# Optimization experiments

Hardware: AMD Instinct MI355X
Metric: run time of the kernel (lower is better)

## Reference

```python
import jax, jax.numpy as jnp
import numpy as np

BD = BH = BW = 4  # block sizes
NH = 8            # num heads


def setup_inputs() -> dict:
    key = jax.random.key(0)
    ks = jax.random.split(key, 5)
    C = 128
    return {
        "x": jax.random.normal(ks[0], (1, C, 30, 62, 126), dtype=jnp.float32),
        "qkv_w": jax.random.normal(ks[1], (3 * C, C), dtype=jnp.float32) * 0.02,
        "qkv_b": jax.random.normal(ks[2], (3 * C,), dtype=jnp.float32) * 0.02,
        "conv_w": jax.random.normal(ks[3], (C, C), dtype=jnp.float32) * 0.02,
        "conv_b": jax.random.normal(ks[4], (C,), dtype=jnp.float32) * 0.02,
    }


def reference(x, qkv_w, qkv_b, conv_w, conv_b):
    B, C, D0, H0, W0 = x.shape
    pad_d = (-D0) % BD
    pad_b = (-H0) % BH
    pad_r = (-W0) % BW
    x = jnp.pad(x, ((0, 0), (0, 0), (0, pad_d), (0, pad_b), (0, pad_r)))
    _, _, D, H, W = x.shape
    d, h, w = D // BD, H // BH, W // BW
    nW, L, hd = d * h * w, BD * BH * BW, C // NH
    scale = hd ** -0.5

    # window partition: (B,C,D,H,W) -> (B, nW, L, C)
    xb = x.reshape(B, C, d, BD, h, BH, w, BW).transpose(0, 2, 4, 6, 3, 5, 7, 1)
    xw = xb.reshape(B, nW, L, C)

    qkv = xw @ qkv_w.T + qkv_b                         # (B,nW,L,3C)
    qkv = qkv.reshape(B, nW, L, 3, NH, hd).transpose(3, 0, 1, 4, 2, 5)
    q, k, v = qkv[0], qkv[1], qkv[2]                   # (B,nW,NH,L,hd)

    attn = jnp.einsum('bnhld,bnhmd->bnhlm', q, k) * scale

    if pad_d > 0 or pad_r > 0 or pad_b > 0:
        mask = jnp.zeros((D, H, W), dtype=x.dtype)
        mask = mask.at[-pad_d:, :, :].set(1.0)
        mask = mask.at[:, -pad_b:, :].set(1.0)
        mask = mask.at[:, :, -pad_r:].set(1.0)
        mask = mask.reshape(d, BD, h, BH, w, BW).transpose(0, 2, 4, 1, 3, 5).reshape(nW, L)
        am = mask[:, None, :] - mask[:, :, None]       # (nW,L,L): mask[j]-mask[i]
        am = jnp.where(am != 0, jnp.asarray(-1000.0, x.dtype), jnp.asarray(0.0, x.dtype))
        attn = attn + am[None, :, None, :, :]

    attn = jax.nn.softmax(attn, axis=-1)
    out = jnp.einsum('bnhlm,bnhmd->bnhld', attn, v)    # (B,nW,NH,L,hd)

    # window merge: -> (B,C,D,H,W)
    out = out.reshape(B, d, h, w, NH, BD, BH, BW, hd)
    out = out.transpose(0, 4, 8, 1, 5, 2, 6, 3, 7).reshape(B, C, D, H, W)
    out = out[:, :, :D0, :H0, :W0]

    # final 1x1x1 conv
    out = jnp.einsum('bcdhw,oc->bodhw', out, conv_w) + conv_b[None, :, None, None, None]
    return out
```

## Files before the change

kernel.cpp:

```cpp
#include <hip/hip_runtime.h>


#define NHEAD 8
#define HDIM 16
#define CCH 128
#define DD0 30
#define HH0 62
#define WW0 126
#define SD 7812
#define SC 234360

typedef __bf16 bfx8 __attribute__((ext_vector_type(8)));
typedef float  fx4  __attribute__((ext_vector_type(4)));
typedef float  fx2  __attribute__((ext_vector_type(2)));

__device__ __forceinline__ fx4 MFMA(bfx8 a, bfx8 b, fx4 c) {
    return __builtin_amdgcn_mfma_f32_16x16x32_bf16(a, b, c, 0, 0, 0);
}
__device__ __forceinline__ fx4 fzero4() { fx4 v = {0.f, 0.f, 0.f, 0.f}; return v; }
__device__ __forceinline__ bfx8 bzero8() {
    bfx8 v;
    #pragma unroll
    for (int j = 0; j < 8; j++) v[j] = (__bf16)0.f;
    return v;
}
__device__ __forceinline__ unsigned pk2(float a, float b) {
    __bf16 ax = (__bf16)a, by = (__bf16)b;
    unsigned short ua = __builtin_bit_cast(unsigned short, ax);
    unsigned short ub = __builtin_bit_cast(unsigned short, by);
    return (unsigned)ua | ((unsigned)ub << 16);
}

__global__ void prep_kernel(const float* __restrict__ qkv_w,
                            const float* __restrict__ conv_w,
                            __bf16* __restrict__ Bq, __bf16* __restrict__ Bc) {
    const int i = blockIdx.x * 256 + threadIdx.x;
    if (i < 49152) Bq[i] = (__bf16)qkv_w[i];
    else            Bc[i - 49152] = (__bf16)conv_w[i - 49152];
}

__global__ __launch_bounds__(256, 4) void winattn_kernel(
    const float* __restrict__ x,
    const float* __restrict__ qkv_b,
    const float* __restrict__ conv_b,
    const __bf16* __restrict__ Bq,
    const __bf16* __restrict__ Bc,
    float* __restrict__ out)
{
    __shared__ __align__(16) unsigned char lds_raw[32768];
    __bf16* ldsQ = (__bf16*)lds_raw;
    __bf16* ldsK = (__bf16*)(lds_raw + 16384);

    const int tid  = threadIdx.x;
    const int wave = tid >> 6;
    const int lane = tid & 63;
    const int quad = lane >> 4;
    const int l15  = lane & 15;

    const int blk = blockIdx.x;
    const int wid = ((blk & 7) << 9) | (blk >> 3);
    const int Db = (wid >> 9) << 2;
    const int Hb = ((wid >> 5) & 15) << 2;
    const int Wb = (wid & 31) << 2;

    unsigned long long pmask;
    {
        const bool p = (Db + (lane >> 4) >= DD0) || (Hb + ((lane >> 2) & 3) >= HH0) ||
                       (Wb + (lane & 3) >= WW0);
        pmask = __ballot(p);
    }

    {
        #pragma unroll
        for (int it = 0; it < 16; it++) {
            const int u = it * 256 + tid;
            const int wp = u & 1;
            const int dh = (u >> 1) & 15;
            const int c  = u >> 5;
            const int Dg = Db + (dh >> 2), Hg = Hb + (dh & 3);
            const bool valid = (Dg < DD0) && (Hg < HH0) && (wp == 0 || Wb < 124);
            fx2 v = {0.f, 0.f};
            if (valid) v = *(const fx2*)(x + c * SC + Dg * SD + Hg * WW0 + Wb + wp * 2);
            const int tok0 = dh * 4 + wp * 2;
            ldsQ[tok0 * 128 + (((c >> 3) ^ (tok0 & 15)) << 3) + (c & 7)] = (__bf16)v[0];
            const int tok1 = tok0 + 1;
            ldsQ[tok1 * 128 + (((c >> 3) ^ (tok1 & 15)) << 3) + (c & 7)] = (__bf16)v[1];
        }
    }
    __syncthreads();

    unsigned vpk[2][4][2];

    {
        fx4 acc[4][4];
        #pragma unroll
        for (int mt = 0; mt < 4; mt++)
            #pragma unroll
            for (int j = 0; j < 4; j++) acc[mt][j] = fzero4();
        #pragma unroll
        for (int ks = 0; ks < 4; ks++) {
            bfx8 a[4];
            #pragma unroll
            for (int mt = 0; mt < 4; mt++) {
                const int m = mt * 16 + l15;
                const int phys = (ks * 4 + quad) ^ (m & 15);
                a[mt] = *(const bfx8*)(ldsQ + m * 128 + phys * 8);
            }
            #pragma unroll
            for (int j = 0; j < 4; j++) {
                const int col = (1 + (j >> 1)) * 128 + (wave + (j & 1) * 4) * 16 + l15;
                const bfx8 bb = *(const bfx8*)(Bq + (col * 16 + ks * 4 + quad) * 8);
                #pragma unroll
                for (int mt = 0; mt < 4; mt++) acc[mt][j] = MFMA(a[mt], bb, acc[mt][j]);
            }
        }
        #pragma unroll
        for (int j = 0; j < 2; j++) {
            const int hh = wave + j * 4;
            const float bias = qkv_b[128 + hh * 16 + l15];
            #pragma unroll
            for (int mt = 0; mt < 4; mt++)
                #pragma unroll
                for (int r = 0; r < 4; r++) {
                    const int tok = mt * 16 + quad * 4 + r;
                    const int phys = (l15 >> 3) ^ ((tok >> 2) & 1);
                    ldsK[hh * 1024 + tok * 16 + phys * 8 + (l15 & 7)] =
                        (__bf16)(acc[mt][j][r] + bias);
                }
        }
        #pragma unroll
        for (int hi = 0; hi < 2; hi++) {
            const float bias = qkv_b[256 + (wave + hi * 4) * 16 + l15];
            #pragma unroll
            for (int mt = 0; mt < 4; mt++) {
                vpk[hi][mt][0] = pk2(acc[mt][2 + hi][0] + bias, acc[mt][2 + hi][1] + bias);
                vpk[hi][mt][1] = pk2(acc[mt][2 + hi][2] + bias, acc[mt][2 + hi][3] + bias);
            }
        }
    }

    {
        fx4 acc[4][2];
        #pragma unroll
        for (int mt = 0; mt < 4; mt++)
            #pragma unroll
            for (int hi = 0; hi < 2; hi++) acc[mt][hi] = fzero4();
        #pragma unroll
        for (int ks = 0; ks < 4; ks++) {
            bfx8 a[4];
            #pragma unroll
            for (int mt = 0; mt < 4; mt++) {
                const int m = mt * 16 + l15;
                const int phys = (ks * 4 + quad) ^ (m & 15);
                a[mt] = *(const bfx8*)(ldsQ + m * 128 + phys * 8);
            }
            #pragma unroll
            for (int hi = 0; hi < 2; hi++) {
                const int col = (wave + hi * 4) * 16 + l15;
                const bfx8 bb = *(const bfx8*)(Bq + (col * 16 + ks * 4 + quad) * 8);
                #pragma unroll
                for (int mt = 0; mt < 4; mt++) acc[mt][hi] = MFMA(a[mt], bb, acc[mt][hi]);
            }
        }
        __syncthreads();
        #pragma unroll
        for (int hi = 0; hi < 2; hi++) {
            const int hh = wave + hi * 4;
            const float bias = qkv_b[hh * 16 + l15];
            #pragma unroll
            for (int mt = 0; mt < 4; mt++)
                #pragma unroll
                for (int r = 0; r < 4; r++) {
                    const int tok = mt * 16 + quad * 4 + r;
                    const int phys = (l15 >> 3) ^ ((tok >> 2) & 1);
                    ldsQ[hh * 1024 + tok * 16 + phys * 8 + (l15 & 7)] =
                        (__bf16)((acc[mt][hi][r] + bias) * 0.25f);
                }
        }
    }
    __syncthreads();

    const int srcA = ((((quad << 1) + 0) & 3) << 4) | l15;
    const int srcB = ((((quad << 1) + 1) & 3) << 4) | l15;
    #pragma unroll
    for (int hi = 0; hi < 2; hi++) {
        const int hh = wave + hi * 4;
        __bf16* qs = ldsQ + hh * 1024;
        __bf16* kk = ldsK + hh * 1024;

        fx4 lg[4][4];
        #pragma unroll
        for (int mt = 0; mt < 4; mt++)
            #pragma unroll
            for (int nt = 0; nt < 4; nt++) lg[mt][nt] = fzero4();

        bfx8 aq[4];
        #pragma unroll
        for (int mt = 0; mt < 4; mt++) {
            aq[mt] = bzero8();
            if (quad < 2) {
                const int m = mt * 16 + l15;
                const int phys = quad ^ ((m >> 2) & 1);
                aq[mt] = *(const bfx8*)(qs + m * 16 + phys * 8);
            }
        }
        #pragma unroll
        for (int nt = 0; nt < 4; nt++) {
            bfx8 bk = bzero8();
            if (quad < 2) {
                const int n = nt * 16 + l15;
                const int phys = quad ^ ((n >> 2) & 1);
                bk = *(const bfx8*)(kk + n * 16 + phys * 8);
            }
            #pragma unroll
            for (int mt = 0; mt < 4; mt++) lg[mt][nt] = MFMA(aq[mt], bk, lg[mt][nt]);
        }

        #pragma unroll
        for (int mt = 0; mt < 4; mt++) {
            float sum[4] = {0.f, 0.f, 0.f, 0.f};
            #pragma unroll
            for (int nt = 0; nt < 4; nt++) {
                const unsigned cb = (unsigned)(pmask >> (nt * 16 + l15)) & 1u;
                #pragma unroll
                for (int r = 0; r < 4; r++) {
                    const unsigned rb = (unsigned)(pmask >> (mt * 16 + quad * 4 + r)) & 1u;
                    const float e = (rb ^ cb) ? 0.f : __expf(lg[mt][nt][r]);
                    lg[mt][nt][r] = e;
                    sum[r] += e;
                }
            }
            #pragma unroll
            for (int r = 0; r < 4; r++) {
                float s = sum[r];
                s += __shfl_xor(s, 1);
                s += __shfl_xor(s, 2);
                s += __shfl_xor(s, 4);
                s += __shfl_xor(s, 8);
                const float rinv = __builtin_amdgcn_rcpf(s);
                #pragma unroll
                for (int nt = 0; nt < 4; nt++) lg[mt][nt][r] *= rinv;
            }
        }

        fx4 ovec[4];
        #pragma unroll
        for (int mt = 0; mt < 4; mt++) ovec[mt] = fzero4();
        #pragma unroll
        for (int half = 0; half < 2; half++) {
            #pragma unroll
            for (int nn = 0; nn < 2; nn++) {
                __bf16* piece = nn ? kk : qs;
                const int nt = half * 2 + nn;
                #pragma unroll
                for (int mt = 0; mt < 4; mt++)
                    #pragma unroll
                    for (int r = 0; r < 4; r++) {
                        const int tok = mt * 16 + quad * 4 + r;
                        const int phys = (l15 >> 3) ^ ((tok >> 2) & 1);
                        piece[tok * 16 + phys * 8 + (l15 & 7)] = (__bf16)lg[mt][nt][r];
                    }
            }
            const unsigned a00 = (unsigned)__shfl((int)vpk[hi][half * 2 + 0][0], srcA);
            const unsigned a01 = (unsigned)__shfl((int)vpk[hi][half * 2 + 0][1], srcA);
            const unsigned a10 = (unsigned)__shfl((int)vpk[hi][half * 2 + 1][0], srcA);
            const unsigned a11 = (unsigned)__shfl((int)vpk[hi][half * 2 + 1][1], srcA);
            const unsigned b00 = (unsigned)__shfl((int)vpk[hi][half * 2 + 0][0], srcB);
            const unsigned b01 = (unsigned)__shfl((int)vpk[hi][half * 2 + 0][1], srcB);
            const unsigned b10 = (unsigned)__shfl((int)vpk[hi][half * 2 + 1][0], srcB);
            const unsigned b11 = (unsigned)__shfl((int)vpk[hi][half * 2 + 1][1], srcB);
            const bool mhi = quad >= 2;
            uint4 uv;
            uv.x = mhi ? a10 : a00;
            uv.y = mhi ? a11 : a01;
            uv.z = mhi ? b10 : b00;
            uv.w = mhi ? b11 : b01;
            const bfx8 bv = __builtin_bit_cast(bfx8, uv);
            #pragma unroll
            for (int mt = 0; mt < 4; mt++) {
                const int m = mt * 16 + l15;
                const int phys = (quad & 1) ^ ((m >> 2) & 1);
                const bfx8 ap = *(const bfx8*)(((quad >> 1) ? kk : qs) + m * 16 + phys * 8);
                ovec[mt] = MFMA(ap, bv, ovec[mt]);
            }
        }
        #pragma unroll
        for (int mt = 0; mt < 4; mt++)
            #pragma unroll
            for (int r = 0; r < 4; r++) {
                const int tok = mt * 16 + quad * 4 + r;
                const int phys = (l15 >> 3) ^ ((tok >> 2) & 1);
                qs[tok * 16 + phys * 8 + (l15 & 7)] = (__bf16)ovec[mt][r];
            }
    }
    __syncthreads();

    {
        fx4 cacc[4][2];
        #pragma unroll
        for (int mt = 0; mt < 4; mt++)
            #pragma unroll
            for (int nt = 0; nt < 2; nt++) cacc[mt][nt] = fzero4();
        #pragma unroll
        for (int ks = 0; ks < 4; ks++) {
            const int kg = ks * 4 + quad;
            bfx8 a[4];
            #pragma unroll
            for (int mt = 0; mt < 4; mt++) {
                const int m = mt * 16 + l15;
                const int phys = (kg & 1) ^ ((m >> 2) & 1);
                a[mt] = *(const bfx8*)(ldsQ + (kg >> 1) * 1024 + m * 16 + phys * 8);
            }
            #pragma unroll
            for (int nt = 0; nt < 2; nt++) {
                const int o = wave * 32 + nt * 16 + l15;
                const bfx8 bb = *(const bfx8*)(Bc + (o * 16 + kg) * 8);
                #pragma unroll
                for (int mt = 0; mt < 4; mt++) cacc[mt][nt] = MFMA(a[mt], bb, cacc[mt][nt]);
            }
        }
        #pragma unroll
        for (int nt = 0; nt < 2; nt++) {
            const int o = wave * 32 + nt * 16 + l15;
            const float cb = conv_b[o];
            #pragma unroll
            for (int mt = 0; mt < 4; mt++) {
                if (Db + mt < DD0) {
                    const int Hg = Hb + quad;
                    if (Hg < HH0) {
                        const int base = o * SC + (Db + mt) * SD + Hg * WW0 + Wb;
                        fx2 w0 = {cacc[mt][nt][0] + cb, cacc[mt][nt][1] + cb};
                        *(fx2*)(out + base) = w0;
                        if (Wb < 124) {
                            fx2 w1 = {cacc[mt][nt][2] + cb, cacc[mt][nt][3] + cb};
                            *(fx2*)(out + base + 2) = w1;
                        }
                    }
                }
            }
        }
    }
}

extern "C" void kernel_launch(void* const* d_in, const int* in_sizes, int n_in,
                              void* d_out, int out_size, void* d_ws, size_t ws_size,
                              hipStream_t stream) {
    const float* x      = (const float*)d_in[0];
    const float* qkv_w  = (const float*)d_in[1];
    const float* qkv_b  = (const float*)d_in[2];
    const float* conv_w = (const float*)d_in[3];
    const float* conv_b = (const float*)d_in[4];
    float* out = (float*)d_out;

    __bf16* Bq = (__bf16*)d_ws;
    __bf16* Bc = (__bf16*)((char*)d_ws + 98304);

    prep_kernel<<<256, 256, 0, stream>>>(qkv_w, conv_w, Bq, Bc);
    winattn_kernel<<<4096, 256, 0, stream>>>(x, qkv_b, conv_b, Bq, Bc, out);
}
```

Before: 440.4 us.

## Restructure window attention softmax: transposed logits, deferred normalization, wider loads

Computes the logits transposed (K as the A operand) so that each lane holds a column of exp values. The row sum is then reduced with two cross-quad shuffles, and normalization is deferred to the PV output instead of rescaling every probability. Exp values are packed to bf16 and written to LDS as 64-bit stores, a branch skips masking for windows with no padding, and the x load uses 4-wide loads per thread with half as many iterations. It also drops one __syncthreads and raises the occupancy hint to 5 blocks, which risks register pressure and spills.

```diff
diff --git a/kernel.cpp b/kernel.cpp
--- a/kernel.cpp
+++ b/kernel.cpp
@@ -39,7 +39,7 @@
     else            Bc[i - 49152] = (__bf16)conv_w[i - 49152];
 }
 
-__global__ __launch_bounds__(256, 4) void winattn_kernel(
+__global__ __launch_bounds__(256, 5) void winattn_kernel(
     const float* __restrict__ x,
     const float* __restrict__ qkv_b,
     const float* __restrict__ conv_b,
@@ -69,22 +69,27 @@
                        (Wb + (lane & 3) >= WW0);
         pmask = __ballot(p);
     }
+    const bool anypad = (pmask != 0ULL);
 
     {
         #pragma unroll
-        for (int it = 0; it < 16; it++) {
+        for (int it = 0; it < 8; it++) {
             const int u = it * 256 + tid;
-            const int wp = u & 1;
-            const int dh = (u >> 1) & 15;
-            const int c  = u >> 5;
+            const int dh = u & 15;
+            const int c  = u >> 4;
             const int Dg = Db + (dh >> 2), Hg = Hb + (dh & 3);
-            const bool valid = (Dg < DD0) && (Hg < HH0) && (wp == 0 || Wb < 124);
-            fx2 v = {0.f, 0.f};
-            if (valid) v = *(const fx2*)(x + c * SC + Dg * SD + Hg * WW0 + Wb + wp * 2);
-            const int tok0 = dh * 4 + wp * 2;
-            ldsQ[tok0 * 128 + (((c >> 3) ^ (tok0 & 15)) << 3) + (c & 7)] = (__bf16)v[0];
-            const int tok1 = tok0 + 1;
-            ldsQ[tok1 * 128 + (((c >> 3) ^ (tok1 & 15)) << 3) + (c & 7)] = (__bf16)v[1];
+            fx2 v0 = {0.f, 0.f}, v1 = {0.f, 0.f};
+            if ((Dg < DD0) && (Hg < HH0)) {
+                const float* px = x + c * SC + Dg * SD + Hg * WW0 + Wb;
+                v0 = *(const fx2*)px;
+                if (Wb < 124) v1 = *(const fx2*)(px + 2);
+            }
+            const int t0 = dh * 4;
+            const int ch = c >> 3, cl = c & 7;
+            ldsQ[(t0 + 0) * 128 + ((ch ^ ((t0 + 0) & 15)) << 3) + cl] = (__bf16)v0[0];
+            ldsQ[(t0 + 1) * 128 + ((ch ^ ((t0 + 1) & 15)) << 3) + cl] = (__bf16)v0[1];
+            ldsQ[(t0 + 2) * 128 + ((ch ^ ((t0 + 2) & 15)) << 3) + cl] = (__bf16)v1[0];
+            ldsQ[(t0 + 3) * 128 + ((ch ^ ((t0 + 3) & 15)) << 3) + cl] = (__bf16)v1[1];
         }
     }
     __syncthreads();
@@ -178,88 +183,131 @@
                 }
         }
     }
-    __syncthreads();
 
     const int srcA = ((((quad << 1) + 0) & 3) << 4) | l15;
     const int srcB = ((((quad << 1) + 1) & 3) << 4) | l15;
+    const int rsrc = lane & 48;
     #pragma unroll
     for (int hi = 0; hi < 2; hi++) {
         const int hh = wave + hi * 4;
         __bf16* qs = ldsQ + hh * 1024;
         __bf16* kk = ldsK + hh * 1024;
 
-        fx4 lg[4][4];
+        bfx8 bq[4];
+        #pragma unroll
+        for (int mt = 0; mt < 4; mt++) {
+            bq[mt] = bzero8();
+            if (quad < 2) {
+                const int m = mt * 16 + l15;
+                const int phys = quad ^ ((m >> 2) & 1);
+                bq[mt] = *(const bfx8*)(qs + m * 16 + phys * 8);
+            }
+        }
+
+        unsigned cb4[4];
         #pragma unroll
         for (int mt = 0; mt < 4; mt++)
-            #pragma unroll
-            for (int nt = 0; nt < 4; nt++) lg[mt][nt] = fzero4();
-
-        bfx8 aq[4];
-        #pragma unroll
-        for (int mt = 0; mt < 4; mt++) {
-            aq[mt] = bzero8();
-            if (quad < 2) {
-                const int m = mt * 16 + l15;
-                const int phys = quad ^ ((m >> 2) & 1);
-                aq[mt] = *(const bfx8*)(qs + m * 16 + phys * 8);
-            }
-        }
-        #pragma unroll
-        for (int nt = 0; nt < 4; nt++) {
-            bfx8 bk = bzero8();
+            cb4[mt] = (unsigned)(pmask >> (mt * 16 + l15)) & 1u;
+
+        float sums[4] = {0.f, 0.f, 0.f, 0.f};
+        unsigned pkS[2][4][2];
+
+        #pragma unroll
+        for (int ntq = 0; ntq < 2; ntq++) {
+            const int nt = 2 + ntq;
+            bfx8 ak = bzero8();
             if (quad < 2) {
                 const int n = nt * 16 + l15;
                 const int phys = quad ^ ((n >> 2) & 1);
-                bk = *(const bfx8*)(kk + n * 16 + phys * 8);
-            }
-            #pragma unroll
-            for (int mt = 0; mt < 4; mt++) lg[mt][nt] = MFMA(aq[mt], bk, lg[mt][nt]);
-        }
-
-        #pragma unroll
-        for (int mt = 0; mt < 4; mt++) {
-            float sum[4] = {0.f, 0.f, 0.f, 0.f};
-            #pragma unroll
-            for (int nt = 0; nt < 4; nt++) {
-                const unsigned cb = (unsigned)(pmask >> (nt * 16 + l15)) & 1u;
-                #pragma unroll
-                for (int r = 0; r < 4; r++) {
-                    const unsigned rb = (unsigned)(pmask >> (mt * 16 + quad * 4 + r)) & 1u;
-                    const float e = (rb ^ cb) ? 0.f : __expf(lg[mt][nt][r]);
-                    lg[mt][nt][r] = e;
-                    sum[r] += e;
-                }
-            }
-            #pragma unroll
-            for (int r = 0; r < 4; r++) {
-                float s = sum[r];
-                s += __shfl_xor(s, 1);
-                s += __shfl_xor(s, 2);
-                s += __shfl_xor(s, 4);
-                s += __shfl_xor(s, 8);
-                const float rinv = __builtin_amdgcn_rcpf(s);
-                #pragma unroll
-                for (int nt = 0; nt < 4; nt++) lg[mt][nt][r] *= rinv;
-            }
-        }
-
-        fx4 ovec[4];
-        #pragma unroll
-        for (int mt = 0; mt < 4; mt++) ovec[mt] = fzero4();
-        #pragma unroll
-        for (int half = 0; half < 2; half++) {
-            #pragma unroll
-            for (int nn = 0; nn < 2; nn++) {
-                __bf16* piece = nn ? kk : qs;
-                const int nt = half * 2 + nn;
-                #pragma unroll
-                for (int mt = 0; mt < 4; mt++)
+                ak = *(const bfx8*)(kk + n * 16 + phys * 8);
+            }
+            fx4 lt[4];
+            #pragma unroll
+            for (int mt = 0; mt < 4; mt++) lt[mt] = MFMA(ak, bq[mt], fzero4());
+            const unsigned rb4 = (unsigned)(pmask >> (nt * 16 + quad * 4));
+            #pragma unroll
+            for (int mt = 0; mt < 4; mt++) {
+                fx4 e;
+                if (anypad) {
                     #pragma unroll
                     for (int r = 0; r < 4; r++) {
-                        const int tok = mt * 16 + quad * 4 + r;
-                        const int phys = (l15 >> 3) ^ ((tok >> 2) & 1);
-                        piece[tok * 16 + phys * 8 + (l15 & 7)] = (__bf16)lg[mt][nt][r];
+                        const unsigned msk = ((rb4 >> r) ^ cb4[mt]) & 1u;
+                        e[r] = msk ? 0.f : __expf(lt[mt][r]);
                     }
+                } else {
+                    #pragma unroll
+                    for (int r = 0; r < 4; r++) e[r] = __expf(lt[mt][r]);
+                }
+                sums[mt] += (e[0] + e[1]) + (e[2] + e[3]);
+                pkS[ntq][mt][0] = pk2(e[0], e[1]);
+                pkS[ntq][mt][1] = pk2(e[2], e[3]);
+            }
+        }
+        #pragma unroll
+        for (int nt = 0; nt < 2; nt++) {
+            bfx8 ak = bzero8();
+            if (quad < 2) {
+                const int n = nt * 16 + l15;
+                const int phys = quad ^ ((n >> 2) & 1);
+                ak = *(const bfx8*)(kk + n * 16 + phys * 8);
+            }
+            fx4 lt[4];
+            #pragma unroll
+            for (int mt = 0; mt < 4; mt++) lt[mt] = MFMA(ak, bq[mt], fzero4());
+            const unsigned rb4 = (unsigned)(pmask >> (nt * 16 + quad * 4));
+            __bf16* piece = nt ? kk : qs;
+            #pragma unroll
+            for (int mt = 0; mt < 4; mt++) {
+                fx4 e;
+                if (anypad) {
+                    #pragma unroll
+                    for (int r = 0; r < 4; r++) {
+                        const unsigned msk = ((rb4 >> r) ^ cb4[mt]) & 1u;
+                        e[r] = msk ? 0.f : __expf(lt[mt][r]);
+                    }
+                } else {
+                    #pragma unroll
+                    for (int r = 0; r < 4; r++) e[r] = __expf(lt[mt][r]);
+                }
+                sums[mt] += (e[0] + e[1]) + (e[2] + e[3]);
+                const int m = mt * 16 + l15;
+                const int addr = m * 16 + (((quad >> 1) ^ ((m >> 2) & 1)) << 3) +
+                                 ((quad & 1) << 2);
+                uint2 wv;
+                wv.x = pk2(e[0], e[1]);
+                wv.y = pk2(e[2], e[3]);
+                *(uint2*)(piece + addr) = wv;
+            }
+        }
+
+        #pragma unroll
+        for (int mt = 0; mt < 4; mt++) {
+            float s = sums[mt];
+            s += __shfl_xor(s, 16);
+            s += __shfl_xor(s, 32);
+            sums[mt] = __builtin_amdgcn_rcpf(s);
+        }
+
+        fx4 ovec[4];
+        #pragma unroll
+        for (int mt = 0; mt < 4; mt++) ovec[mt] = fzero4();
+        #pragma unroll
+        for (int half = 0; half < 2; half++) {
+            if (half == 1) {
+                #pragma unroll
+                for (int ntq = 0; ntq < 2; ntq++) {
+                    __bf16* piece = ntq ? kk : qs;
+                    #pragma unroll
+                    for (int mt = 0; mt < 4; mt++) {
+                        const int m = mt * 16 + l15;
+                        const int addr = m * 16 + (((quad >> 1) ^ ((m >> 2) & 1)) << 3) +
+                                         ((quad & 1) << 2);
+                        uint2 wv;
+                        wv.x = pkS[ntq][mt][0];
+                        wv.y = pkS[ntq][mt][1];
+                        *(uint2*)(piece + addr) = wv;
+                    }
+                }
             }
             const unsigned a00 = (unsigned)__shfl((int)vpk[hi][half * 2 + 0][0], srcA);
             const unsigned a01 = (unsigned)__shfl((int)vpk[hi][half * 2 + 0][1], srcA);
@@ -288,9 +336,10 @@
         for (int mt = 0; mt < 4; mt++)
             #pragma unroll
             for (int r = 0; r < 4; r++) {
+                const float rv = __shfl(sums[mt], rsrc | (quad * 4 + r));
                 const int tok = mt * 16 + quad * 4 + r;
                 const int phys = (l15 >> 3) ^ ((tok >> 2) & 1);
-                qs[tok * 16 + phys * 8 + (l15 & 7)] = (__bf16)ovec[mt][r];
+                qs[tok * 16 + phys * 8 + (l15 & 7)] = (__bf16)(ovec[mt][r] * rv);
             }
     }
     __syncthreads();
@@ -346,10 +395,10 @@
                               void* d_out, int out_size, void* d_ws, size_t ws_size,
                               hipStream_t stream) {
     const float* x      = (const float*)d_in[0];
+    const float* qkv_b  = (const float*)d_in[2];
+    const float* conv_b = (const float*)d_in[4];
     const float* qkv_w  = (const float*)d_in[1];
-    const float* qkv_b  = (const float*)d_in[2];
     const float* conv_w = (const float*)d_in[3];
-    const float* conv_b = (const float*)d_in[4];
     float* out = (float*)d_out;
 
     __bf16* Bq = (__bf16*)d_ws;
```

Result: slower. 502.4 us (+14.1%).

## Split QKV projection into per-operand passes and defer softmax normalization

Applied to the files above, without the earlier changes.

Computes Q, V and K projections in three separate passes with a smaller accumulator set, reordering LDS region use so one barrier can be dropped. The softmax is restructured to compute logits per column tile, fold log2(e) into the Q scale so it can use exp2, skip the mask logic for windows with no padding, and normalize the output after P·V instead of normalizing the probabilities. The launch bound rises to 5 waves-per-SIMD target to push occupancy. The cost is re-reading the input tile from LDS three times and extra packed-register state for the deferred probability tiles.

```diff
diff --git a/kernel.cpp b/kernel.cpp
--- a/kernel.cpp
+++ b/kernel.cpp
@@ -9,6 +9,7 @@
 #define WW0 126
 #define SD 7812
 #define SC 234360
+#define QSCALE 0.3606737602f
 
 typedef __bf16 bfx8 __attribute__((ext_vector_type(8)));
 typedef float  fx4  __attribute__((ext_vector_type(4)));
@@ -39,7 +40,7 @@
     else            Bc[i - 49152] = (__bf16)conv_w[i - 49152];
 }
 
-__global__ __launch_bounds__(256, 4) void winattn_kernel(
+__global__ __launch_bounds__(256, 5) void winattn_kernel(
     const float* __restrict__ x,
     const float* __restrict__ qkv_b,
     const float* __restrict__ conv_b,
@@ -48,8 +49,8 @@
     float* __restrict__ out)
 {
     __shared__ __align__(16) unsigned char lds_raw[32768];
-    __bf16* ldsQ = (__bf16*)lds_raw;
-    __bf16* ldsK = (__bf16*)(lds_raw + 16384);
+    __bf16* R0 = (__bf16*)lds_raw;
+    __bf16* R1 = (__bf16*)(lds_raw + 16384);
 
     const int tid  = threadIdx.x;
     const int wave = tid >> 6;
@@ -69,6 +70,7 @@
                        (Wb + (lane & 3) >= WW0);
         pmask = __ballot(p);
     }
+    const bool anypad = (pmask != 0ULL);
 
     {
         #pragma unroll
@@ -82,9 +84,10 @@
             fx2 v = {0.f, 0.f};
             if (valid) v = *(const fx2*)(x + c * SC + Dg * SD + Hg * WW0 + Wb + wp * 2);
             const int tok0 = dh * 4 + wp * 2;
-            ldsQ[tok0 * 128 + (((c >> 3) ^ (tok0 & 15)) << 3) + (c & 7)] = (__bf16)v[0];
+            const int ch = c >> 3, cl = c & 7;
+            R0[tok0 * 128 + ((ch ^ (tok0 & 15)) << 3) + cl] = (__bf16)v[0];
             const int tok1 = tok0 + 1;
-            ldsQ[tok1 * 128 + (((c >> 3) ^ (tok1 & 15)) << 3) + (c & 7)] = (__bf16)v[1];
+            R0[tok1 * 128 + ((ch ^ (tok1 & 15)) << 3) + cl] = (__bf16)v[1];
         }
     }
     __syncthreads();
@@ -92,11 +95,11 @@
     unsigned vpk[2][4][2];
 
     {
-        fx4 acc[4][4];
-        #pragma unroll
-        for (int mt = 0; mt < 4; mt++)
-            #pragma unroll
-            for (int j = 0; j < 4; j++) acc[mt][j] = fzero4();
+        fx4 acc[4][2];
+        #pragma unroll
+        for (int mt = 0; mt < 4; mt++)
+            #pragma unroll
+            for (int hi = 0; hi < 2; hi++) acc[mt][hi] = fzero4();
         #pragma unroll
         for (int ks = 0; ks < 4; ks++) {
             bfx8 a[4];
@@ -104,37 +107,62 @@
             for (int mt = 0; mt < 4; mt++) {
                 const int m = mt * 16 + l15;
                 const int phys = (ks * 4 + quad) ^ (m & 15);
-                a[mt] = *(const bfx8*)(ldsQ + m * 128 + phys * 8);
-            }
-            #pragma unroll
-            for (int j = 0; j < 4; j++) {
-                const int col = (1 + (j >> 1)) * 128 + (wave + (j & 1) * 4) * 16 + l15;
+                a[mt] = *(const bfx8*)(R0 + m * 128 + phys * 8);
+            }
+            #pragma unroll
+            for (int hi = 0; hi < 2; hi++) {
+                const int col = (wave + hi * 4) * 16 + l15;
                 const bfx8 bb = *(const bfx8*)(Bq + (col * 16 + ks * 4 + quad) * 8);
                 #pragma unroll
-                for (int mt = 0; mt < 4; mt++) acc[mt][j] = MFMA(a[mt], bb, acc[mt][j]);
-            }
-        }
-        #pragma unroll
-        for (int j = 0; j < 2; j++) {
-            const int hh = wave + j * 4;
-            const float bias = qkv_b[128 + hh * 16 + l15];
+                for (int mt = 0; mt < 4; mt++) acc[mt][hi] = MFMA(a[mt], bb, acc[mt][hi]);
+            }
+        }
+        #pragma unroll
+        for (int hi = 0; hi < 2; hi++) {
+            const int hh = wave + hi * 4;
+            const float bias = qkv_b[hh * 16 + l15];
             #pragma unroll
             for (int mt = 0; mt < 4; mt++)
                 #pragma unroll
                 for (int r = 0; r < 4; r++) {
                     const int tok = mt * 16 + quad * 4 + r;
                     const int phys = (l15 >> 3) ^ ((tok >> 2) & 1);
-                    ldsK[hh * 1024 + tok * 16 + phys * 8 + (l15 & 7)] =
-                        (__bf16)(acc[mt][j][r] + bias);
-                }
+                    R1[hh * 1024 + tok * 16 + phys * 8 + (l15 & 7)] =
+                        (__bf16)((acc[mt][hi][r] + bias) * QSCALE);
+                }
+        }
+    }
+
+    {
+        fx4 acc[4][2];
+        #pragma unroll
+        for (int mt = 0; mt < 4; mt++)
+            #pragma unroll
+            for (int hi = 0; hi < 2; hi++) acc[mt][hi] = fzero4();
+        #pragma unroll
+        for (int ks = 0; ks < 4; ks++) {
+            bfx8 a[4];
+            #pragma unroll
+            for (int mt = 0; mt < 4; mt++) {
+                const int m = mt * 16 + l15;
+                const int phys = (ks * 4 + quad) ^ (m & 15);
+                a[mt] = *(const bfx8*)(R0 + m * 128 + phys * 8);
+            }
+            #pragma unroll
+            for (int hi = 0; hi < 2; hi++) {
+                const int col = 256 + (wave + hi * 4) * 16 + l15;
+                const bfx8 bb = *(const bfx8*)(Bq + (col * 16 + ks * 4 + quad) * 8);
+                #pragma unroll
+                for (int mt = 0; mt < 4; mt++) acc[mt][hi] = MFMA(a[mt], bb, acc[mt][hi]);
+            }
         }
         #pragma unroll
         for (int hi = 0; hi < 2; hi++) {
             const float bias = qkv_b[256 + (wave + hi * 4) * 16 + l15];
             #pragma unroll
             for (int mt = 0; mt < 4; mt++) {
-                vpk[hi][mt][0] = pk2(acc[mt][2 + hi][0] + bias, acc[mt][2 + hi][1] + bias);
-                vpk[hi][mt][1] = pk2(acc[mt][2 + hi][2] + bias, acc[mt][2 + hi][3] + bias);
+                vpk[hi][mt][0] = pk2(acc[mt][hi][0] + bias, acc[mt][hi][1] + bias);
+                vpk[hi][mt][1] = pk2(acc[mt][hi][2] + bias, acc[mt][hi][3] + bias);
             }
         }
     }
@@ -152,11 +180,11 @@
             for (int mt = 0; mt < 4; mt++) {
                 const int m = mt * 16 + l15;
                 const int phys = (ks * 4 + quad) ^ (m & 15);
-                a[mt] = *(const bfx8*)(ldsQ + m * 128 + phys * 8);
+                a[mt] = *(const bfx8*)(R0 + m * 128 + phys * 8);
             }
             #pragma unroll
             for (int hi = 0; hi < 2; hi++) {
-                const int col = (wave + hi * 4) * 16 + l15;
+                const int col = 128 + (wave + hi * 4) * 16 + l15;
                 const bfx8 bb = *(const bfx8*)(Bq + (col * 16 + ks * 4 + quad) * 8);
                 #pragma unroll
                 for (int mt = 0; mt < 4; mt++) acc[mt][hi] = MFMA(a[mt], bb, acc[mt][hi]);
@@ -166,33 +194,26 @@
         #pragma unroll
         for (int hi = 0; hi < 2; hi++) {
             const int hh = wave + hi * 4;
-            const float bias = qkv_b[hh * 16 + l15];
+            const float bias = qkv_b[128 + hh * 16 + l15];
             #pragma unroll
             for (int mt = 0; mt < 4; mt++)
                 #pragma unroll
                 for (int r = 0; r < 4; r++) {
                     const int tok = mt * 16 + quad * 4 + r;
                     const int phys = (l15 >> 3) ^ ((tok >> 2) & 1);
-                    ldsQ[hh * 1024 + tok * 16 + phys * 8 + (l15 & 7)] =
-                        (__bf16)((acc[mt][hi][r] + bias) * 0.25f);
-                }
-        }
-    }
-    __syncthreads();
+                    R0[hh * 1024 + tok * 16 + phys * 8 + (l15 & 7)] =
+                        (__bf16)(acc[mt][hi][r] + bias);
+                }
+        }
+    }
 
     const int srcA = ((((quad << 1) + 0) & 3) << 4) | l15;
     const int srcB = ((((quad << 1) + 1) & 3) << 4) | l15;
     #pragma unroll
     for (int hi = 0; hi < 2; hi++) {
         const int hh = wave + hi * 4;
-        __bf16* qs = ldsQ + hh * 1024;
-        __bf16* kk = ldsK + hh * 1024;
-
-        fx4 lg[4][4];
-        #pragma unroll
-        for (int mt = 0; mt < 4; mt++)
-            #pragma unroll
-            for (int nt = 0; nt < 4; nt++) lg[mt][nt] = fzero4();
+        __bf16* qs = R1 + hh * 1024;
+        __bf16* kk = R0 + hh * 1024;
 
         bfx8 aq[4];
         #pragma unroll
@@ -204,62 +225,111 @@
                 aq[mt] = *(const bfx8*)(qs + m * 16 + phys * 8);
             }
         }
-        #pragma unroll
-        for (int nt = 0; nt < 4; nt++) {
+
+        float part[4][4];
+        #pragma unroll
+        for (int mt = 0; mt < 4; mt++)
+            #pragma unroll
+            for (int r = 0; r < 4; r++) part[mt][r] = 0.f;
+
+        unsigned pkS[2][4][2];
+
+        #pragma unroll
+        for (int ntq = 0; ntq < 2; ntq++) {
+            const int nt = 2 + ntq;
             bfx8 bk = bzero8();
             if (quad < 2) {
                 const int n = nt * 16 + l15;
                 const int phys = quad ^ ((n >> 2) & 1);
                 bk = *(const bfx8*)(kk + n * 16 + phys * 8);
             }
-            #pragma unroll
-            for (int mt = 0; mt < 4; mt++) lg[mt][nt] = MFMA(aq[mt], bk, lg[mt][nt]);
-        }
-
-        #pragma unroll
-        for (int mt = 0; mt < 4; mt++) {
-            float sum[4] = {0.f, 0.f, 0.f, 0.f};
-            #pragma unroll
-            for (int nt = 0; nt < 4; nt++) {
-                const unsigned cb = (unsigned)(pmask >> (nt * 16 + l15)) & 1u;
-                #pragma unroll
-                for (int r = 0; r < 4; r++) {
-                    const unsigned rb = (unsigned)(pmask >> (mt * 16 + quad * 4 + r)) & 1u;
-                    const float e = (rb ^ cb) ? 0.f : __expf(lg[mt][nt][r]);
-                    lg[mt][nt][r] = e;
-                    sum[r] += e;
-                }
-            }
-            #pragma unroll
-            for (int r = 0; r < 4; r++) {
-                float s = sum[r];
-                s += __shfl_xor(s, 1);
-                s += __shfl_xor(s, 2);
-                s += __shfl_xor(s, 4);
-                s += __shfl_xor(s, 8);
-                const float rinv = __builtin_amdgcn_rcpf(s);
-                #pragma unroll
-                for (int nt = 0; nt < 4; nt++) lg[mt][nt][r] *= rinv;
-            }
-        }
-
-        fx4 ovec[4];
-        #pragma unroll
-        for (int mt = 0; mt < 4; mt++) ovec[mt] = fzero4();
-        #pragma unroll
-        for (int half = 0; half < 2; half++) {
-            #pragma unroll
-            for (int nn = 0; nn < 2; nn++) {
-                __bf16* piece = nn ? kk : qs;
-                const int nt = half * 2 + nn;
-                #pragma unroll
-                for (int mt = 0; mt < 4; mt++)
+            fx4 lt[4];
+            #pragma unroll
+            for (int mt = 0; mt < 4; mt++) lt[mt] = MFMA(aq[mt], bk, fzero4());
+            const unsigned cb = (unsigned)(pmask >> (nt * 16 + l15)) & 1u;
+            #pragma unroll
+            for (int mt = 0; mt < 4; mt++) {
+                fx4 e;
+                if (anypad) {
                     #pragma unroll
                     for (int r = 0; r < 4; r++) {
-                        const int tok = mt * 16 + quad * 4 + r;
-                        const int phys = (l15 >> 3) ^ ((tok >> 2) & 1);
-                        piece[tok * 16 + phys * 8 + (l15 & 7)] = (__bf16)lg[mt][nt][r];
+                        const unsigned rb =
+                            (unsigned)(pmask >> (mt * 16 + quad * 4 + r)) & 1u;
+                        e[r] = (rb ^ cb) ? 0.f : __builtin_amdgcn_exp2f(lt[mt][r]);
                     }
+                } else {
+                    #pragma unroll
+                    for (int r = 0; r < 4; r++)
+                        e[r] = __builtin_amdgcn_exp2f(lt[mt][r]);
+                }
+                #pragma unroll
+                for (int r = 0; r < 4; r++) part[mt][r] += e[r];
+                pkS[ntq][mt][0] = pk2(e[0], e[1]);
+                pkS[ntq][mt][1] = pk2(e[2], e[3]);
+            }
+        }
+        #pragma unroll
+        for (int nt = 0; nt < 2; nt++) {
+            bfx8 bk = bzero8();
+            if (quad < 2) {
+                const int n = nt * 16 + l15;
+                const int phys = quad ^ ((n >> 2) & 1);
+                bk = *(const bfx8*)(kk + n * 16 + phys * 8);
+            }
+            fx4 lt[4];
+            #pragma unroll
+            for (int mt = 0; mt < 4; mt++) lt[mt] = MFMA(aq[mt], bk, fzero4());
+            __bf16* piece = nt ? kk : qs;
+            const unsigned cb = (unsigned)(pmask >> (nt * 16 + l15)) & 1u;
+            #pragma unroll
+            for (int mt = 0; mt < 4; mt++) {
+                fx4 e;
+                if (anypad) {
+                    #pragma unroll
+                    for (int r = 0; r < 4; r++) {
+                        const unsigned rb =
+                            (unsigned)(pmask >> (mt * 16 + quad * 4 + r)) & 1u;
+                        e[r] = (rb ^ cb) ? 0.f : __builtin_amdgcn_exp2f(lt[mt][r]);
+                    }
+                } else {
+                    #pragma unroll
+                    for (int r = 0; r < 4; r++)
+                        e[r] = __builtin_amdgcn_exp2f(lt[mt][r]);
+                }
+                #pragma unroll
+                for (int r = 0; r < 4; r++) {
+                    part[mt][r] += e[r];
+                    const int tok = mt * 16 + quad * 4 + r;
+                    const int phys = (l15 >> 3) ^ ((tok >> 2) & 1);
+                    piece[tok * 16 + phys * 8 + (l15 & 7)] = (__bf16)e[r];
+                }
+            }
+        }
+
+        fx4 ovec[4];
+        #pragma unroll
+        for (int mt = 0; mt < 4; mt++) ovec[mt] = fzero4();
+
+        #pragma unroll
+        for (int half = 0; half < 2; half++) {
+            if (half == 1) {
+                #pragma unroll
+                for (int ntq = 0; ntq < 2; ntq++) {
+                    __bf16* piece = ntq ? kk : qs;
+                    #pragma unroll
+                    for (int mt = 0; mt < 4; mt++)
+                        #pragma unroll
+                        for (int r = 0; r < 4; r++) {
+                            const unsigned pr = pkS[ntq][mt][r >> 1];
+                            const unsigned short hv =
+                                (r & 1) ? (unsigned short)(pr >> 16)
+                                        : (unsigned short)(pr & 0xffffu);
+                            const int tok = mt * 16 + quad * 4 + r;
+                            const int phys = (l15 >> 3) ^ ((tok >> 2) & 1);
+                            piece[tok * 16 + phys * 8 + (l15 & 7)] =
+                                __builtin_bit_cast(__bf16, hv);
+                        }
+                }
             }
             const unsigned a00 = (unsigned)__shfl((int)vpk[hi][half * 2 + 0][0], srcA);
             const unsigned a01 = (unsigned)__shfl((int)vpk[hi][half * 2 + 0][1], srcA);
@@ -288,9 +358,15 @@
         for (int mt = 0; mt < 4; mt++)
             #pragma unroll
             for (int r = 0; r < 4; r++) {
+                float s = part[mt][r];
+                s += __shfl_xor(s, 1);
+                s += __shfl_xor(s, 2);
+                s += __shfl_xor(s, 4);
+                s += __shfl_xor(s, 8);
+                const float rinv = __builtin_amdgcn_rcpf(s);
                 const int tok = mt * 16 + quad * 4 + r;
                 const int phys = (l15 >> 3) ^ ((tok >> 2) & 1);
-                qs[tok * 16 + phys * 8 + (l15 & 7)] = (__bf16)ovec[mt][r];
+                kk[tok * 16 + phys * 8 + (l15 & 7)] = (__bf16)(ovec[mt][r] * rinv);
             }
     }
     __syncthreads();
@@ -309,7 +385,7 @@
             for (int mt = 0; mt < 4; mt++) {
                 const int m = mt * 16 + l15;
                 const int phys = (kg & 1) ^ ((m >> 2) & 1);
-                a[mt] = *(const bfx8*)(ldsQ + (kg >> 1) * 1024 + m * 16 + phys * 8);
+                a[mt] = *(const bfx8*)(R0 + (kg >> 1) * 1024 + m * 16 + phys * 8);
             }
             #pragma unroll
             for (int nt = 0; nt < 2; nt++) {
```

Result: slower. 721.2 us (+63.7%).
